# Kernel optimization log

Measured on AMD Instinct MI355X. Metric: run time of the kernel, lower is better.

Reference implementation:

```python
import jax, jax.numpy as jnp
import numpy as np

MAX_ITER = 20
F_TOL = 1e-6
FREE_NUM = 64  # free_idx[1] + 1
TRUNC = (0, 512)  # truncate_idx


def setup_inputs() -> dict:
    key = jax.random.key(0)
    ks = jax.random.split(key, 8)
    bsz, in_dim, hid, out_dim, m = 1024, 512, 1024, 256, 128
    return {
        "b_primal": jax.random.normal(ks[0], (bsz, in_dim), jnp.float32),
        "W0": jax.random.normal(ks[1], (hid, in_dim), jnp.float32) / np.sqrt(in_dim).astype(np.float32),
        "b0": jnp.zeros((hid,), jnp.float32),
        "W1": jax.random.normal(ks[2], (hid, hid), jnp.float32) / np.sqrt(hid).astype(np.float32),
        "b1": jnp.zeros((hid,), jnp.float32),
        "W2": jax.random.normal(ks[3], (out_dim, hid), jnp.float32) / np.sqrt(hid).astype(np.float32),
        "b2": jnp.zeros((out_dim,), jnp.float32),
        "A": jax.random.normal(ks[4], (m, out_dim), jnp.float32) * 0.1,
        "b_vec": jax.random.normal(ks[5], (m,), jnp.float32),
        # scaled so spectral norm < 1 -> contracting fixed-point iteration
        "WzProj": jax.random.normal(ks[6], (out_dim, out_dim), jnp.float32) * 0.03,
        "WbProj": jax.random.normal(ks[7], (out_dim, m), jnp.float32) * 0.1,
    }


def reference(b_primal, W0, b0, W1, b1, W2, b2, A, b_vec, WzProj, WbProj):
    # eval-mode forward of DualNN (report_projection=True)
    x = b_primal[:, TRUNC[0]:TRUNC[1]]
    h = jax.nn.relu(x @ W0.T + b0)
    h = jax.nn.relu(h @ W1.T + b1)
    out = h @ W2.T + b2                      # [bsz, output_dim]

    bias_proj = b_vec @ WbProj.T             # [output_dim]

    def cond(state):
        _, it, res = state
        return (it <= MAX_ITER) & (res > F_TOL)

    def body(state):
        z, it, _ = state
        z = bias_proj + z @ WzProj.T         # affine projection step
        u = z[:, :FREE_NUM]
        v = jax.nn.relu(z[:, FREE_NUM:])     # clamp non-free coordinates
        z = jnp.concatenate([u, v], axis=-1)
        res = jnp.max(jnp.abs(z @ A.T - b_vec))  # inf-norm equality residual
        return z, it + 1, res

    z_star, curr_iter, _ = jax.lax.while_loop(
        cond, body, (out, jnp.int32(1), jnp.float32(jnp.inf)))
    return (z_star, out, curr_iter)
```

## Files before the change

### kernel.cpp

```cpp
#include <hip/hip_runtime.h>

typedef __attribute__((ext_vector_type(8))) __bf16 bf16x8;
typedef __attribute__((ext_vector_type(4))) float f32x4;

#define MAX_ITER_N 20
#define F_TOL_F 1e-6f
#define FREE_NUM_N 64

#define BSZ 1024
#define IN_DIM 512
#define HID 1024
#define OUT_DIM 256
#define M_CON 128

#define WS_BAR   0
#define WS_RES   8
#define WS_BP    48
#define WS_H1    304
#define WS_H2    (WS_H1 + 524288)
#define WS_APC   (WS_H2 + 524288)
#define WS_W0C   (WS_APC + 262144)
#define WS_W1C   (WS_W0C + 262144)
#define WS_W2C   (WS_W1C + 524288)
#define WS_WZG   (WS_W2C + 131072)
#define WS_AG    (WS_WZG + 32768)

__device__ __forceinline__ unsigned short f2bf(float f) {
    unsigned int u = __float_as_uint(f);
    u += 0x7fffu + ((u >> 16) & 1u);
    return (unsigned short)(u >> 16);
}

__device__ __forceinline__ void gload_lds16(const unsigned short* g, unsigned short* l) {
    __builtin_amdgcn_global_load_lds(
        (const __attribute__((address_space(1))) unsigned int*)(const void*)g,
        (__attribute__((address_space(3))) unsigned int*)(void*)l, 16, 0, 0);
}

__global__ __launch_bounds__(256) void prep_k(
    const float* __restrict__ b_primal, const float* __restrict__ W0,
    const float* __restrict__ W1, const float* __restrict__ W2,
    const float* __restrict__ Wz, const float* __restrict__ Am,
    const float* __restrict__ b_vec, const float* __restrict__ WbProj,
    float* __restrict__ ws)
{
    unsigned short* APc = (unsigned short*)(ws + WS_APC);
    unsigned short* W0c = (unsigned short*)(ws + WS_W0C);
    unsigned short* W1c = (unsigned short*)(ws + WS_W1C);
    unsigned short* W2c = (unsigned short*)(ws + WS_W2C);
    unsigned short* WzG = (unsigned short*)(ws + WS_WZG);
    unsigned short* AG  = (unsigned short*)(ws + WS_AG);
    float* bp = ws + WS_BP;

    int b = blockIdx.x;
    int tid = threadIdx.x;
    if (b >= 2400) {
        float s = 0.0f;
        for (int k = 0; k < M_CON; ++k) s += b_vec[k] * WbProj[tid * M_CON + k];
        bp[tid] = s;
        return;
    }
    const float* src; unsigned short* dst; int off;
    if (b < 512)       { src = b_primal; dst = APc; off = b; }
    else if (b < 1024) { src = W0; dst = W0c; off = b - 512; }
    else if (b < 2048) { src = W1; dst = W1c; off = b - 1024; }
    else if (b < 2304) { src = W2; dst = W2c; off = b - 2048; }
    else if (b < 2368) { src = Wz; dst = WzG; off = b - 2304; }
    else               { src = Am; dst = AG;  off = b - 2368; }
    int idx = off * 1024 + tid * 4;
    float4 v = *(const float4*)(src + idx);
    ushort4 o;
    o.x = f2bf(v.x); o.y = f2bf(v.y); o.z = f2bf(v.z); o.w = f2bf(v.w);
    *(ushort4*)(dst + idx) = o;
}

__device__ __forceinline__ bf16x8 frag128(const unsigned short* lds, int row, int gc) {
    int phys = gc ^ (row & 15);
    return __builtin_bit_cast(bf16x8, *(const uint4*)(lds + row * 128 + phys * 8));
}

template<int K, int NTN, bool RELU, bool F32OUT>
__global__ __launch_bounds__(256, 4) void gemm32_k(
    const unsigned short* __restrict__ A,
    const unsigned short* __restrict__ B,
    const float* __restrict__ bias,
    void* __restrict__ Cv, int N_)
{
    constexpr int NCH = K / 128;
    __shared__ __align__(16) unsigned short As[2][32 * 128];
    __shared__ __align__(16) unsigned short Bs[2][32 * 128];

    const int tid = threadIdx.x;
    const int w = tid >> 6;
    const int lane = tid & 63;
    const int ln = lane & 15;
    const int q  = lane >> 4;
    const int wr = w >> 1;
    const int wc = w & 1;
    const int row0 = (blockIdx.x / NTN) * 32;
    const int col0 = (blockIdx.x % NTN) * 32;
    const unsigned short* Ab = A + row0 * K;
    const unsigned short* Bb = B + col0 * K;

    int soff[2], dbase[2];
#pragma unroll
    for (int i = 0; i < 2; ++i) {
        int P = w * 128 + i * 64 + lane;
        int row = P >> 4, pgc = P & 15;
        soff[i]  = row * K + (pgc ^ (row & 15)) * 8;
        dbase[i] = (w * 128 + i * 64) * 8;
    }

    f32x4 acc = {0.f, 0.f, 0.f, 0.f};

#pragma unroll
    for (int i = 0; i < 2; ++i) {
        gload_lds16(Ab + soff[i], &As[0][dbase[i]]);
        gload_lds16(Bb + soff[i], &Bs[0][dbase[i]]);
    }

    for (int c = 0; c < NCH; ++c) {
        __syncthreads();
        if (c + 1 < NCH) {
            const unsigned short* Ak = Ab + (c + 1) * 128;
            const unsigned short* Bk = Bb + (c + 1) * 128;
            int nb = (c + 1) & 1;
#pragma unroll
            for (int i = 0; i < 2; ++i) {
                gload_lds16(Ak + soff[i], &As[nb][dbase[i]]);
                gload_lds16(Bk + soff[i], &Bs[nb][dbase[i]]);
            }
        }
        const unsigned short* Ac = As[c & 1];
        const unsigned short* Bc = Bs[c & 1];
#pragma unroll
        for (int ks = 0; ks < 4; ++ks) {
            bf16x8 af = frag128(Ac, wr * 16 + ln, ks * 4 + q);
            bf16x8 bf = frag128(Bc, wc * 16 + ln, ks * 4 + q);
            acc = __builtin_amdgcn_mfma_f32_16x16x32_bf16(af, bf, acc, 0, 0, 0);
        }
    }

    const int c = col0 + wc * 16 + ln;
    const float bv = bias[c];
#pragma unroll
    for (int i = 0; i < 4; ++i) {
        int r = row0 + wr * 16 + q * 4 + i;
        float v = acc[i] + bv;
        if (RELU) v = fmaxf(v, 0.0f);
        if (F32OUT) ((float*)Cv)[r * N_ + c] = v;
        else ((unsigned short*)Cv)[r * N_ + c] = f2bf(v);
    }
}

__global__ __launch_bounds__(256, 1) void loop_k(
    const float* __restrict__ b_vec, float* __restrict__ out,
    float* __restrict__ ws)
{
    __shared__ __align__(16) unsigned char smem[16 * 264 * 2 + 256];
    unsigned int* res = (unsigned int*)(ws + WS_RES);
    float* bp = ws + WS_BP;
    const unsigned short* WzG = (const unsigned short*)(ws + WS_WZG);
    const unsigned short* AG  = (const unsigned short*)(ws + WS_AG);
    float* outz = out + BSZ * OUT_DIM;

    const int tid  = threadIdx.x;
    const int wave = tid >> 6;
    const int lane = tid & 63;
    const int ln   = lane & 15;
    const int q    = lane >> 4;
    const int r0   = blockIdx.x * 16;

    unsigned short (*zS)[264] = (unsigned short(*)[264])smem;
    float* red = (float*)(smem + 16 * 264 * 2);

    {
        int row = tid >> 4;
        int c0  = (tid & 15) * 16;
        const float* src = outz + (r0 + row) * OUT_DIM + c0;
#pragma unroll
        for (int i = 0; i < 16; ++i) zS[row][c0 + i] = f2bf(src[i]);
    }

    bf16x8 afr[2][8];
    float bvv[2];
#pragma unroll
    for (int mt = 0; mt < 2; ++mt) {
        int m = wave * 32 + mt * 16 + ln;
        bvv[mt] = b_vec[m];
#pragma unroll
        for (int ks = 0; ks < 8; ++ks)
            afr[mt][ks] = __builtin_bit_cast(bf16x8, *(const uint4*)(AG + m * OUT_DIM + ks * 32 + q * 8));
    }
    int colg[4];
    float bpv[4];
    bf16x8 wzfr[4][8];
#pragma unroll
    for (int nt = 0; nt < 4; ++nt) {
        colg[nt] = wave * 64 + nt * 16 + ln;
        bpv[nt]  = bp[colg[nt]];
#pragma unroll
        for (int ks = 0; ks < 8; ++ks)
            wzfr[nt][ks] = __builtin_bit_cast(bf16x8, *(const uint4*)(WzG + colg[nt] * OUT_DIM + ks * 32 + q * 8));
    }
    __syncthreads();

    bf16x8 zfr[8];
#pragma unroll
    for (int ks = 0; ks < 8; ++ks)
        zfr[ks] = __builtin_bit_cast(bf16x8, *(const uint4*)&zS[ln][ks * 32 + q * 8]);

    const f32x4 zero4 = {0.f, 0.f, 0.f, 0.f};

    for (int t = 1; t <= MAX_ITER_N; ++t) {
        f32x4 acc[4];
#pragma unroll
        for (int nt = 0; nt < 4; ++nt) acc[nt] = zero4;
#pragma unroll
        for (int ks = 0; ks < 8; ++ks)
#pragma unroll
            for (int nt = 0; nt < 4; ++nt)
                acc[nt] = __builtin_amdgcn_mfma_f32_16x16x32_bf16(zfr[ks], wzfr[nt][ks], acc[nt], 0, 0, 0);
        float vals[4][4];
#pragma unroll
        for (int nt = 0; nt < 4; ++nt)
#pragma unroll
            for (int i = 0; i < 4; ++i) {
                float v = acc[nt][i] + bpv[nt];
                if (colg[nt] >= FREE_NUM_N) v = fmaxf(v, 0.0f);
                vals[nt][i] = v;
            }
        if (t == MAX_ITER_N) {
#pragma unroll
            for (int nt = 0; nt < 4; ++nt)
#pragma unroll
                for (int i = 0; i < 4; ++i)
                    out[(r0 + q * 4 + i) * OUT_DIM + colg[nt]] = vals[nt][i];
        }
        __syncthreads();
#pragma unroll
        for (int nt = 0; nt < 4; ++nt)
#pragma unroll
            for (int i = 0; i < 4; ++i)
                zS[q * 4 + i][colg[nt]] = f2bf(vals[nt][i]);
        __syncthreads();
#pragma unroll
        for (int ks = 0; ks < 8; ++ks)
            zfr[ks] = __builtin_bit_cast(bf16x8, *(const uint4*)&zS[ln][ks * 32 + q * 8]);

        f32x4 acc2[2];
        acc2[0] = zero4; acc2[1] = zero4;
#pragma unroll
        for (int ks = 0; ks < 8; ++ks)
#pragma unroll
            for (int mt = 0; mt < 2; ++mt)
                acc2[mt] = __builtin_amdgcn_mfma_f32_16x16x32_bf16(zfr[ks], afr[mt][ks], acc2[mt], 0, 0, 0);
        float lmax = 0.0f;
#pragma unroll
        for (int mt = 0; mt < 2; ++mt)
#pragma unroll
            for (int i = 0; i < 4; ++i)
                lmax = fmaxf(lmax, fabsf(acc2[mt][i] - bvv[mt]));
#pragma unroll
        for (int off = 32; off > 0; off >>= 1)
            lmax = fmaxf(lmax, __shfl_xor(lmax, off));
        if (lane == 0) red[wave] = lmax;
        __syncthreads();
        if (tid == 0) {
            float bm = fmaxf(fmaxf(red[0], red[1]), fmaxf(red[2], red[3]));
            atomicMax(res + (t - 1), __float_as_uint(bm));
        }
    }
}

__global__ __launch_bounds__(256) void decide_fb_k(
    const float* __restrict__ WzProj, float* __restrict__ out,
    float* __restrict__ ws)
{
    __shared__ float zF[16][257];
    unsigned int* res = (unsigned int*)(ws + WS_RES);
    float* bp = ws + WS_BP;
    float* outz = out + BSZ * OUT_DIM;
    const int tid = threadIdx.x;

    int T = MAX_ITER_N;
    for (int t = 0; t < MAX_ITER_N; ++t) {
        float r = __uint_as_float(res[t]);
        if (!(r > F_TOL_F)) { T = t + 1; break; }
    }
    if (blockIdx.x == 0 && tid == 0)
        out[2 * BSZ * OUT_DIM] = (float)(T + 1);

    if (T >= MAX_ITER_N) return;

    const int r0 = blockIdx.x * 16;
    const int row = tid >> 4;
    const int c0 = (tid & 15) * 16;
    for (int i = 0; i < 16; ++i) zF[row][c0 + i] = outz[(r0 + row) * OUT_DIM + c0 + i];
    __syncthreads();
    const int j = tid;
    const float bj = bp[j];
    for (int t = 0; t < T; ++t) {
        float acc[16] = {};
        for (int k = 0; k < OUT_DIM; ++k) {
            float w = WzProj[j * OUT_DIM + k];
#pragma unroll
            for (int r = 0; r < 16; ++r) acc[r] += zF[r][k] * w;
        }
        __syncthreads();
#pragma unroll
        for (int r = 0; r < 16; ++r) {
            float v = acc[r] + bj;
            if (j >= FREE_NUM_N) v = fmaxf(v, 0.0f);
            zF[r][j] = v;
        }
        __syncthreads();
    }
    for (int i = 0; i < 16; ++i) out[(r0 + row) * OUT_DIM + c0 + i] = zF[row][c0 + i];
}

extern "C" void kernel_launch(void* const* d_in, const int* in_sizes, int n_in,
                              void* d_out, int out_size, void* d_ws, size_t ws_size,
                              hipStream_t stream) {
    const float* b_primal = (const float*)d_in[0];
    const float* W0     = (const float*)d_in[1];
    const float* b0     = (const float*)d_in[2];
    const float* W1     = (const float*)d_in[3];
    const float* b1     = (const float*)d_in[4];
    const float* W2     = (const float*)d_in[5];
    const float* b2     = (const float*)d_in[6];
    const float* Amat   = (const float*)d_in[7];
    const float* b_vec  = (const float*)d_in[8];
    const float* WzProj = (const float*)d_in[9];
    const float* WbProj = (const float*)d_in[10];
    float* out = (float*)d_out;
    float* ws  = (float*)d_ws;

    unsigned short* h1c = (unsigned short*)(ws + WS_H1);
    unsigned short* h2c = (unsigned short*)(ws + WS_H2);
    unsigned short* APc = (unsigned short*)(ws + WS_APC);
    unsigned short* W0c = (unsigned short*)(ws + WS_W0C);
    unsigned short* W1c = (unsigned short*)(ws + WS_W1C);
    unsigned short* W2c = (unsigned short*)(ws + WS_W2C);
    float* outz = out + BSZ * OUT_DIM;

    hipMemsetAsync(ws, 0, WS_BP * sizeof(float), stream);

    hipLaunchKernelGGL(prep_k, dim3(2401), dim3(256), 0, stream,
                       b_primal, W0, W1, W2, WzProj, Amat, b_vec, WbProj, ws);

    hipLaunchKernelGGL((gemm32_k<IN_DIM, 32, true, false>), dim3(1024), dim3(256), 0, stream,
                       APc, W0c, b0, (void*)h1c, HID);
    hipLaunchKernelGGL((gemm32_k<HID, 32, true, false>), dim3(1024), dim3(256), 0, stream,
                       h1c, W1c, b1, (void*)h2c, HID);
    hipLaunchKernelGGL((gemm32_k<HID, 8, false, true>), dim3(256), dim3(256), 0, stream,
                       h2c, W2c, b2, (void*)outz, OUT_DIM);

    hipLaunchKernelGGL(loop_k, dim3(64), dim3(256), 0, stream, b_vec, out, ws);
    hipLaunchKernelGGL(decide_fb_k, dim3(64), dim3(256), 0, stream, WzProj, out, ws);
}
```

Before: 141.9 us.

## Fuse fallback into loop kernel, overlap residual MFMAs, use 64x64 GEMM tiles

Several changes land together. The memset is replaced by zeroing inside prep_k, and the two hidden-layer GEMMs switch to a 64x64-tile kernel with a 2x2 MFMA register tile per wave. The loop kernel interleaves the residual MFMAs of the previous iterate with the next projection step, which removes one barrier pair per iteration. The separate decide/fallback kernel is merged into loop_k through a grid-wide atomic spin barrier. These cut launches and per-iteration sync, but the spin barrier assumes all 64 blocks are co-resident, and the larger tiles lower the block count.

Measured after the change: 142.4 us. About the same (+0.4%).

```diff
diff --git a/kernel.cpp b/kernel.cpp
--- a/kernel.cpp
+++ b/kernel.cpp
@@ -55,6 +55,7 @@
     int b = blockIdx.x;
     int tid = threadIdx.x;
     if (b >= 2400) {
+        if (tid < 48) ((unsigned int*)ws)[tid] = 0u;
         float s = 0.0f;
         for (int k = 0; k < M_CON; ++k) s += b_vec[k] * WbProj[tid * M_CON + k];
         bp[tid] = s;
@@ -80,6 +81,95 @@
 }
 
 template<int K, int NTN, bool RELU, bool F32OUT>
+__global__ __launch_bounds__(256, 2) void gemm64_k(
+    const unsigned short* __restrict__ A,
+    const unsigned short* __restrict__ B,
+    const float* __restrict__ bias,
+    void* __restrict__ Cv, int N_)
+{
+    constexpr int NCH = K / 128;
+    __shared__ __align__(16) unsigned short As[2][64 * 128];
+    __shared__ __align__(16) unsigned short Bs[2][64 * 128];
+
+    const int tid = threadIdx.x;
+    const int w = tid >> 6;
+    const int lane = tid & 63;
+    const int ln = lane & 15;
+    const int q  = lane >> 4;
+    const int wr = w >> 1;
+    const int wc = w & 1;
+    const int row0 = (blockIdx.x / NTN) * 64;
+    const int col0 = (blockIdx.x % NTN) * 64;
+    const unsigned short* Ab = A + row0 * K;
+    const unsigned short* Bb = B + col0 * K;
+
+    int soff[4], dbase[4];
+#pragma unroll
+    for (int i = 0; i < 4; ++i) {
+        int P = w * 256 + i * 64 + lane;
+        int row = P >> 4, pgc = P & 15;
+        soff[i]  = row * K + (pgc ^ (row & 15)) * 8;
+        dbase[i] = (w * 256 + i * 64) * 8;
+    }
+
+    f32x4 acc[2][2];
+#pragma unroll
+    for (int rm = 0; rm < 2; ++rm)
+#pragma unroll
+        for (int cn = 0; cn < 2; ++cn)
+            acc[rm][cn] = (f32x4){0.f, 0.f, 0.f, 0.f};
+
+#pragma unroll
+    for (int i = 0; i < 4; ++i) {
+        gload_lds16(Ab + soff[i], &As[0][dbase[i]]);
+        gload_lds16(Bb + soff[i], &Bs[0][dbase[i]]);
+    }
+
+    for (int c = 0; c < NCH; ++c) {
+        __syncthreads();
+        if (c + 1 < NCH) {
+            const unsigned short* Ak = Ab + (c + 1) * 128;
+            const unsigned short* Bk = Bb + (c + 1) * 128;
+            int nb = (c + 1) & 1;
+#pragma unroll
+            for (int i = 0; i < 4; ++i) {
+                gload_lds16(Ak + soff[i], &As[nb][dbase[i]]);
+                gload_lds16(Bk + soff[i], &Bs[nb][dbase[i]]);
+            }
+        }
+        const unsigned short* Ac = As[c & 1];
+        const unsigned short* Bc = Bs[c & 1];
+#pragma unroll
+        for (int ks = 0; ks < 4; ++ks) {
+            bf16x8 af0 = frag128(Ac, wr * 32 + ln,      ks * 4 + q);
+            bf16x8 af1 = frag128(Ac, wr * 32 + 16 + ln, ks * 4 + q);
+            bf16x8 bf0 = frag128(Bc, wc * 32 + ln,      ks * 4 + q);
+            bf16x8 bf1 = frag128(Bc, wc * 32 + 16 + ln, ks * 4 + q);
+            acc[0][0] = __builtin_amdgcn_mfma_f32_16x16x32_bf16(af0, bf0, acc[0][0], 0, 0, 0);
+            acc[0][1] = __builtin_amdgcn_mfma_f32_16x16x32_bf16(af0, bf1, acc[0][1], 0, 0, 0);
+            acc[1][0] = __builtin_amdgcn_mfma_f32_16x16x32_bf16(af1, bf0, acc[1][0], 0, 0, 0);
+            acc[1][1] = __builtin_amdgcn_mfma_f32_16x16x32_bf16(af1, bf1, acc[1][1], 0, 0, 0);
+        }
+    }
+
+#pragma unroll
+    for (int cn = 0; cn < 2; ++cn) {
+        const int cc = col0 + wc * 32 + cn * 16 + ln;
+        const float bv = bias[cc];
+#pragma unroll
+        for (int rm = 0; rm < 2; ++rm)
+#pragma unroll
+            for (int i = 0; i < 4; ++i) {
+                int r = row0 + wr * 32 + rm * 16 + q * 4 + i;
+                float v = acc[rm][cn][i] + bv;
+                if (RELU) v = fmaxf(v, 0.0f);
+                if (F32OUT) ((float*)Cv)[r * N_ + cc] = v;
+                else ((unsigned short*)Cv)[r * N_ + cc] = f2bf(v);
+            }
+    }
+}
+
+template<int K, int NTN, bool RELU, bool F32OUT>
 __global__ __launch_bounds__(256, 4) void gemm32_k(
     const unsigned short* __restrict__ A,
     const unsigned short* __restrict__ B,
@@ -154,10 +244,11 @@
 }
 
 __global__ __launch_bounds__(256, 1) void loop_k(
-    const float* __restrict__ b_vec, float* __restrict__ out,
-    float* __restrict__ ws)
+    const float* __restrict__ b_vec, const float* __restrict__ WzProj,
+    float* __restrict__ out, float* __restrict__ ws)
 {
-    __shared__ __align__(16) unsigned char smem[16 * 264 * 2 + 256];
+    __shared__ __align__(16) unsigned char smem[16 * 257 * 4 + 64];
+    unsigned int* done = (unsigned int*)ws;
     unsigned int* res = (unsigned int*)(ws + WS_RES);
     float* bp = ws + WS_BP;
     const unsigned short* WzG = (const unsigned short*)(ws + WS_WZG);
@@ -172,14 +263,19 @@
     const int r0   = blockIdx.x * 16;
 
     unsigned short (*zS)[264] = (unsigned short(*)[264])smem;
-    float* red = (float*)(smem + 16 * 264 * 2);
+    float* red = (float*)(smem + 16 * 257 * 4);
 
     {
         int row = tid >> 4;
         int c0  = (tid & 15) * 16;
         const float* src = outz + (r0 + row) * OUT_DIM + c0;
 #pragma unroll
-        for (int i = 0; i < 16; ++i) zS[row][c0 + i] = f2bf(src[i]);
+        for (int i = 0; i < 4; ++i) {
+            float4 v = *(const float4*)(src + i * 4);
+            ushort4 o;
+            o.x = f2bf(v.x); o.y = f2bf(v.y); o.z = f2bf(v.z); o.w = f2bf(v.w);
+            *(ushort4*)&zS[row][c0 + i * 4] = o;
+        }
     }
 
     bf16x8 afr[2][8];
@@ -214,13 +310,21 @@
 
     for (int t = 1; t <= MAX_ITER_N; ++t) {
         f32x4 acc[4];
+        f32x4 acc2[2];
 #pragma unroll
         for (int nt = 0; nt < 4; ++nt) acc[nt] = zero4;
-#pragma unroll
-        for (int ks = 0; ks < 8; ++ks)
+        acc2[0] = zero4; acc2[1] = zero4;
+#pragma unroll
+        for (int ks = 0; ks < 8; ++ks) {
 #pragma unroll
             for (int nt = 0; nt < 4; ++nt)
                 acc[nt] = __builtin_amdgcn_mfma_f32_16x16x32_bf16(zfr[ks], wzfr[nt][ks], acc[nt], 0, 0, 0);
+            if (t > 1) {
+#pragma unroll
+                for (int mt = 0; mt < 2; ++mt)
+                    acc2[mt] = __builtin_amdgcn_mfma_f32_16x16x32_bf16(zfr[ks], afr[mt][ks], acc2[mt], 0, 0, 0);
+            }
+        }
         float vals[4][4];
 #pragma unroll
         for (int nt = 0; nt < 4; ++nt)
@@ -230,6 +334,18 @@
                 if (colg[nt] >= FREE_NUM_N) v = fmaxf(v, 0.0f);
                 vals[nt][i] = v;
             }
+        if (t > 1) {
+            float lmax = 0.0f;
+#pragma unroll
+            for (int mt = 0; mt < 2; ++mt)
+#pragma unroll
+                for (int i = 0; i < 4; ++i)
+                    lmax = fmaxf(lmax, fabsf(acc2[mt][i] - bvv[mt]));
+#pragma unroll
+            for (int off = 32; off > 0; off >>= 1)
+                lmax = fmaxf(lmax, __shfl_xor(lmax, off));
+            if (lane == 0) red[wave] = lmax;
+        }
         if (t == MAX_ITER_N) {
 #pragma unroll
             for (int nt = 0; nt < 4; ++nt)
@@ -238,6 +354,10 @@
                     out[(r0 + q * 4 + i) * OUT_DIM + colg[nt]] = vals[nt][i];
         }
         __syncthreads();
+        if (t > 1 && tid == 0) {
+            float bm = fmaxf(fmaxf(red[0], red[1]), fmaxf(red[2], red[3]));
+            atomicMax(res + (t - 2), __float_as_uint(bm));
+        }
 #pragma unroll
         for (int nt = 0; nt < 4; ++nt)
 #pragma unroll
@@ -247,7 +367,9 @@
 #pragma unroll
         for (int ks = 0; ks < 8; ++ks)
             zfr[ks] = __builtin_bit_cast(bf16x8, *(const uint4*)&zS[ln][ks * 32 + q * 8]);
-
+    }
+
+    {
         f32x4 acc2[2];
         acc2[0] = zero4; acc2[1] = zero4;
 #pragma unroll
@@ -268,55 +390,59 @@
         __syncthreads();
         if (tid == 0) {
             float bm = fmaxf(fmaxf(red[0], red[1]), fmaxf(red[2], red[3]));
-            atomicMax(res + (t - 1), __float_as_uint(bm));
-        }
-    }
-}
-
-__global__ __launch_bounds__(256) void decide_fb_k(
-    const float* __restrict__ WzProj, float* __restrict__ out,
-    float* __restrict__ ws)
-{
-    __shared__ float zF[16][257];
-    unsigned int* res = (unsigned int*)(ws + WS_RES);
-    float* bp = ws + WS_BP;
-    float* outz = out + BSZ * OUT_DIM;
-    const int tid = threadIdx.x;
-
-    int T = MAX_ITER_N;
-    for (int t = 0; t < MAX_ITER_N; ++t) {
-        float r = __uint_as_float(res[t]);
-        if (!(r > F_TOL_F)) { T = t + 1; break; }
+            atomicMax(res + (MAX_ITER_N - 1), __float_as_uint(bm));
+            __threadfence();
+            atomicAdd(done, 1u);
+            while (__hip_atomic_load(done, __ATOMIC_ACQUIRE, __HIP_MEMORY_SCOPE_AGENT) < 64u)
+                __builtin_amdgcn_s_sleep(2);
+        }
+        __syncthreads();
+    }
+
+    int T;
+    {
+        float rv = 1e30f;
+        if (tid < MAX_ITER_N)
+            rv = __uint_as_float(__hip_atomic_load(res + tid, __ATOMIC_ACQUIRE, __HIP_MEMORY_SCOPE_AGENT));
+        if (tid < 64) {
+            unsigned long long m = __ballot((tid < MAX_ITER_N) && !(rv > F_TOL_F));
+            if (tid == 0) red[0] = (float)(m ? (int)__ffsll(m) : MAX_ITER_N);
+        }
+        __syncthreads();
+        T = (int)red[0];
     }
     if (blockIdx.x == 0 && tid == 0)
         out[2 * BSZ * OUT_DIM] = (float)(T + 1);
-
     if (T >= MAX_ITER_N) return;
 
-    const int r0 = blockIdx.x * 16;
-    const int row = tid >> 4;
-    const int c0 = (tid & 15) * 16;
-    for (int i = 0; i < 16; ++i) zF[row][c0 + i] = outz[(r0 + row) * OUT_DIM + c0 + i];
-    __syncthreads();
-    const int j = tid;
-    const float bj = bp[j];
-    for (int t = 0; t < T; ++t) {
-        float acc[16] = {};
-        for (int k = 0; k < OUT_DIM; ++k) {
-            float w = WzProj[j * OUT_DIM + k];
-#pragma unroll
-            for (int r = 0; r < 16; ++r) acc[r] += zF[r][k] * w;
-        }
-        __syncthreads();
-#pragma unroll
-        for (int r = 0; r < 16; ++r) {
-            float v = acc[r] + bj;
-            if (j >= FREE_NUM_N) v = fmaxf(v, 0.0f);
-            zF[r][j] = v;
-        }
-        __syncthreads();
-    }
-    for (int i = 0; i < 16; ++i) out[(r0 + row) * OUT_DIM + c0 + i] = zF[row][c0 + i];
+    float (*zF)[257] = (float(*)[257])smem;
+    {
+        const int row = tid >> 4;
+        const int c0 = (tid & 15) * 16;
+        for (int i = 0; i < 16; ++i)
+            zF[row][c0 + i] = outz[(r0 + row) * OUT_DIM + c0 + i];
+        __syncthreads();
+        const int j = tid;
+        const float bj = bp[j];
+        for (int t = 0; t < T; ++t) {
+            float acc[16] = {};
+            for (int k = 0; k < OUT_DIM; ++k) {
+                float wv = WzProj[j * OUT_DIM + k];
+#pragma unroll
+                for (int r = 0; r < 16; ++r) acc[r] += zF[r][k] * wv;
+            }
+            __syncthreads();
+#pragma unroll
+            for (int r = 0; r < 16; ++r) {
+                float v = acc[r] + bj;
+                if (j >= FREE_NUM_N) v = fmaxf(v, 0.0f);
+                zF[r][j] = v;
+            }
+            __syncthreads();
+        }
+        for (int i = 0; i < 16; ++i)
+            out[(r0 + row) * OUT_DIM + c0 + i] = zF[row][c0 + i];
+    }
 }
 
 extern "C" void kernel_launch(void* const* d_in, const int* in_sizes, int n_in,
@@ -344,18 +470,15 @@
     unsigned short* W2c = (unsigned short*)(ws + WS_W2C);
     float* outz = out + BSZ * OUT_DIM;
 
-    hipMemsetAsync(ws, 0, WS_BP * sizeof(float), stream);
-
     hipLaunchKernelGGL(prep_k, dim3(2401), dim3(256), 0, stream,
                        b_primal, W0, W1, W2, WzProj, Amat, b_vec, WbProj, ws);
 
-    hipLaunchKernelGGL((gemm32_k<IN_DIM, 32, true, false>), dim3(1024), dim3(256), 0, stream,
+    hipLaunchKernelGGL((gemm64_k<IN_DIM, 16, true, false>), dim3(256), dim3(256), 0, stream,
                        APc, W0c, b0, (void*)h1c, HID);
-    hipLaunchKernelGGL((gemm32_k<HID, 32, true, false>), dim3(1024), dim3(256), 0, stream,
+    hipLaunchKernelGGL((gemm64_k<HID, 16, true, false>), dim3(256), dim3(256), 0, stream,
                        h1c, W1c, b1, (void*)h2c, HID);
     hipLaunchKernelGGL((gemm32_k<HID, 8, false, true>), dim3(256), dim3(256), 0, stream,
                        h2c, W2c, b2, (void*)outz, OUT_DIM);
 
-    hipLaunchKernelGGL(loop_k, dim3(64), dim3(256), 0, stream, b_vec, out, ws);
-    hipLaunchKernelGGL(decide_fb_k, dim3(64), dim3(256), 0, stream, WzProj, out, ws);
-}
+    hipLaunchKernelGGL(loop_k, dim3(64), dim3(256), 0, stream, b_vec, WzProj, out, ws);
+}
```
